# Optimization experiments

Measured on AMD Instinct MI355X. Metric: run time of the kernel, lower is better.

## Reference

```python
import jax, jax.numpy as jnp
import numpy as np

COMMIT_LAMBDA = 0.25


def setup_inputs() -> dict:
    key = jax.random.key(0)
    k1, k2 = jax.random.split(key)
    B, C, T = 8, 256, 1024
    NCB, K, D = 2, 8192, 128
    x = jax.random.normal(k1, (B, C, T), dtype=jnp.float32)
    # EMA codebook weights buffer (init: randn * 0.1)
    codebooks = jax.random.normal(k2, (NCB, K, D), dtype=jnp.float32) * 0.1
    return {"x": x, "codebooks": codebooks}


def reference(x, codebooks):
    B, C, T = x.shape
    ncb, K, d = codebooks.shape
    # [B, C, T] -> [B*T, ncb, d]
    xs = x.reshape(B, ncb, d, T).transpose(0, 3, 1, 2).reshape(B * T, ncb, d)
    # squared euclidean distances (argmin-equivalent to cdist)
    x2 = jnp.sum(xs * xs, axis=-1)[..., None]            # [N, ncb, 1]
    c2 = jnp.sum(codebooks * codebooks, axis=-1)[None]    # [1, ncb, K]
    xc = jnp.einsum('bnd,nkd->bnk', xs, codebooks)        # [N, ncb, K]
    d2 = x2 - 2.0 * xc + c2
    idx = jnp.argmin(d2, axis=-1)                         # [N, ncb] int
    # gather nearest code vectors: [N, ncb, d]
    q = codebooks[jnp.arange(ncb)[None, :], idx]
    # straight-through estimator
    q_st = xs + jax.lax.stop_gradient(q - xs)
    # commitment loss (training mode): sum over codebooks of mse(x_i, q_i.detach())
    loss = COMMIT_LAMBDA * jnp.sum(
        jnp.mean((xs - jax.lax.stop_gradient(q)) ** 2, axis=(0, 2))
    )
    # reassemble to [B, C, T]
    quantized = q_st.reshape(B, T, ncb, d).transpose(0, 2, 3, 1).reshape(B, C, T)
    indices = idx.reshape(B, T, ncb).transpose(0, 2, 1)   # [B, ncb, T]
    return quantized, indices, loss
```

## Files before the change

### kernel.cpp

```cpp
#include <hip/hip_runtime.h>
#include <hip/hip_bf16.h>

#define BB   8
#define TT   1024
#define NCBN 2
#define DD   128
#define KK   8192
#define MM   8192

constexpr int OUT_IDX_OFF  = BB * 256 * TT;
constexpr int OUT_LOSS_OFF = OUT_IDX_OFF + BB * NCBN * TT;

#define THR   0.45f
#define QCAP  768

typedef __attribute__((ext_vector_type(8))) short   short8;
typedef __attribute__((ext_vector_type(4))) float   float4v;

__device__ __forceinline__ unsigned short f2bf(float v) {
    unsigned u = __float_as_uint(v);
    return (unsigned short)((u + 0x7FFFu + ((u >> 16) & 1u)) >> 16);
}

__device__ __forceinline__ void gl_lds16(const void* g, void* l) {
    __builtin_amdgcn_global_load_lds(
        (const __attribute__((address_space(1))) unsigned int*)g,
        (__attribute__((address_space(3))) unsigned int*)l, 16, 0, 0);
}

__global__ __launch_bounds__(256)
void pack_x_kernel(const float* __restrict__ x, unsigned short* __restrict__ xbf,
                   float* __restrict__ x2, unsigned long long* __restrict__ pmin) {
    __shared__ float Ld[DD][65];
    const int b = blockIdx.x >> 1, n = blockIdx.x & 1;
    const int t0 = blockIdx.y * 64;
    const int tid = threadIdx.x;

    const float* base = x + ((size_t)(b * 256 + n * 128)) * TT + t0;
    const int dro = tid >> 2, q4 = tid & 3;
#pragma unroll
    for (int half = 0; half < 2; ++half) {
        int d = dro + half * 64;
        const float* rp = base + (size_t)d * TT + q4 * 16;
#pragma unroll
        for (int j = 0; j < 4; ++j) {
            float4 v = *(const float4*)(rp + j * 4);
            int t = q4 * 16 + j * 4;
            Ld[d][t + 0] = v.x; Ld[d][t + 1] = v.y;
            Ld[d][t + 2] = v.z; Ld[d][t + 3] = v.w;
        }
    }
    __syncthreads();

    if (tid < 64) {
        float s = 0.f;
        for (int d = 0; d < DD; ++d) { float v = Ld[d][tid]; s = fmaf(v, v, s); }
        x2[(size_t)n * MM + b * TT + t0 + tid] = s;
        pmin[(size_t)n * MM + b * TT + t0 + tid] = 0xFFFFFFFFFFFFFFFFull;
    }

    unsigned short* orow0 = xbf + ((size_t)n * MM + b * TT + t0) * DD;
#pragma unroll
    for (int pp = 0; pp < 4; ++pp) {
        int u = tid + pp * 256;
        int tt = u >> 4, sg = u & 15;
        unsigned short tmp[8];
#pragma unroll
        for (int j = 0; j < 8; ++j) tmp[j] = f2bf(Ld[sg * 8 + j][tt]);
        uint4 pk;
        pk.x = (unsigned)tmp[0] | ((unsigned)tmp[1] << 16);
        pk.y = (unsigned)tmp[2] | ((unsigned)tmp[3] << 16);
        pk.z = (unsigned)tmp[4] | ((unsigned)tmp[5] << 16);
        pk.w = (unsigned)tmp[6] | ((unsigned)tmp[7] << 16);
        *(uint4*)(orow0 + (size_t)tt * DD + sg * 8) = pk;
    }
}

__global__ __launch_bounds__(256)
void pack_c_kernel(const float* __restrict__ cb, unsigned short* __restrict__ cbf,
                   float* __restrict__ c2, float* __restrict__ out) {
    int g = blockIdx.x * 256 + threadIdx.x;
    if (g == 0) out[OUT_LOSS_OFF] = 0.f;
    const float4* crow = (const float4*)(cb + (size_t)g * DD);
    unsigned short* orow = cbf + (size_t)g * DD;
    float s = 0.f;
#pragma unroll 4
    for (int i2 = 0; i2 < 16; ++i2) {
        float4 v0 = crow[2 * i2];
        float4 v1 = crow[2 * i2 + 1];
        s = fmaf(v0.x, v0.x, s); s = fmaf(v0.y, v0.y, s);
        s = fmaf(v0.z, v0.z, s); s = fmaf(v0.w, v0.w, s);
        s = fmaf(v1.x, v1.x, s); s = fmaf(v1.y, v1.y, s);
        s = fmaf(v1.z, v1.z, s); s = fmaf(v1.w, v1.w, s);
        uint4 pk;
        pk.x = (unsigned)f2bf(v0.x) | ((unsigned)f2bf(v0.y) << 16);
        pk.y = (unsigned)f2bf(v0.z) | ((unsigned)f2bf(v0.w) << 16);
        pk.z = (unsigned)f2bf(v1.x) | ((unsigned)f2bf(v1.y) << 16);
        pk.w = (unsigned)f2bf(v1.z) | ((unsigned)f2bf(v1.w) << 16);
        *(uint4*)(orow + i2 * 8) = pk;
    }
    c2[g] = s;
}

__device__ void rescore_one(int n, int m, int k,
                            const float* __restrict__ x, const float* __restrict__ cb,
                            const float* __restrict__ x2, const float* __restrict__ c2,
                            unsigned long long* __restrict__ pmin) {
    int b = m >> 10, t = m & (TT - 1);
    const float* xp = x + ((size_t)(b * 256 + n * 128)) * TT + t;
    const float* cp = cb + ((size_t)(n * KK + k)) * DD;
    float xc = 0.f;
    for (int d = 0; d < DD; ++d)
        xc = fmaf(xp[(size_t)d * TT], cp[d], xc);
    float u = x2[n * MM + m] - 2.0f * xc;
    float s = u + c2[n * KK + k];
    unsigned long long pk = ((unsigned long long)__float_as_uint(s) << 32) | (unsigned)k;
    atomicMin(pmin + (size_t)n * MM + m, pk);
}

__global__ __launch_bounds__(256, 2)
void screen_kernel(const unsigned short* __restrict__ xbf,
                   const unsigned short* __restrict__ cbf,
                   const float* __restrict__ c2,
                   const float* __restrict__ x,
                   const float* __restrict__ cb32,
                   const float* __restrict__ x2,
                   unsigned long long* __restrict__ pmin) {
    __shared__ __align__(16) unsigned short Qsh[128 * 128];
    __shared__ __align__(16) unsigned short Ash[128 * 128];
    __shared__ unsigned int   minU[128];
    __shared__ float          c2s[128];
    __shared__ unsigned int   qcnt;
    __shared__ unsigned int   queue[QCAP];

    const int tid = threadIdx.x;
    const int id  = blockIdx.x;
    const int n   = id & 1;
    const int ks  = (id >> 1) & 3;
    const int qt  = id >> 3;
    const int m0  = qt * 128;
    const int k0  = ks * 2048;

    const int wave = tid >> 6, lane = tid & 63;
    const int cw = wave & 1, qw = wave >> 1;
    const int quad = lane >> 4, l15 = lane & 15;

    int goff[8];
#pragma unroll
    for (int p = 0; p < 8; ++p) {
        int u   = (p * 4 + wave) * 64 + lane;
        int row = u >> 4;
        int seg = (u & 15) ^ (row & 15);
        goff[p] = (row * DD + seg * 8) * 2;
    }

    {
        const char* src = (const char*)(xbf + ((size_t)n * MM + m0) * DD);
#pragma unroll
        for (int p = 0; p < 8; ++p)
            gl_lds16(src + goff[p], &Qsh[(p * 4 + wave) * 512]);
    }
    if (tid < 128) minU[tid] = 0xFFFFFFFFu;
    if (tid == 0)  qcnt = 0;
    __syncthreads();

    short8 bfr[4][4];
#pragma unroll
    for (int tq = 0; tq < 4; ++tq) {
        int q = qw * 64 + tq * 16 + l15;
#pragma unroll
        for (int k4 = 0; k4 < 4; ++k4) {
            int seg = k4 * 4 + quad;
            bfr[tq][k4] = *(const short8*)(&Qsh[q * 128 + ((seg ^ l15) * 8)]);
        }
    }

    float mloc[4] = {3.4e38f, 3.4e38f, 3.4e38f, 3.4e38f};
    float thr[4]  = {3.4e38f, 3.4e38f, 3.4e38f, 3.4e38f};

    const char*  asrc0 = (const char*)(cbf + ((size_t)n * KK + k0) * DD);
    const float* c2p   = c2 + (size_t)n * KK + k0;

#pragma unroll
    for (int phase = 0; phase < 2; ++phase) {
        for (int ch = 0; ch < 16; ++ch) {
            __syncthreads();
            {
                const char* src = asrc0 + (size_t)ch * (128 * DD * 2);
#pragma unroll
                for (int p = 0; p < 8; ++p)
                    gl_lds16(src + goff[p], &Ash[(p * 4 + wave) * 512]);
                if (tid < 32)
                    *(float4*)&c2s[tid * 4] =
                        *(const float4*)(c2p + ch * 128 + tid * 4);
            }
            __syncthreads();

            float4v acc[4][4];
#pragma unroll
            for (int tc = 0; tc < 4; ++tc)
#pragma unroll
                for (int tq = 0; tq < 4; ++tq)
                    acc[tc][tq] = (float4v){0.f, 0.f, 0.f, 0.f};

#pragma unroll
            for (int k4 = 0; k4 < 4; ++k4) {
                short8 a[4];
#pragma unroll
                for (int tc = 0; tc < 4; ++tc) {
                    int r = cw * 64 + tc * 16 + l15;
                    int seg = k4 * 4 + quad;
                    a[tc] = *(const short8*)(&Ash[r * 128 + ((seg ^ l15) * 8)]);
                }
#pragma unroll
                for (int tc = 0; tc < 4; ++tc)
#pragma unroll
                    for (int tq = 0; tq < 4; ++tq)
                        acc[tc][tq] = __builtin_amdgcn_mfma_f32_16x16x32_bf16(
                            a[tc], bfr[tq][k4], acc[tc][tq], 0, 0, 0);
            }

#pragma unroll
            for (int tc = 0; tc < 4; ++tc) {
                float4v c2r = *(const float4v*)(&c2s[cw * 64 + tc * 16 + quad * 4]);
#pragma unroll
                for (int tq = 0; tq < 4; ++tq) {
                    float y0 = fmaf(-2.0f, acc[tc][tq][0], c2r[0]);
                    float y1 = fmaf(-2.0f, acc[tc][tq][1], c2r[1]);
                    float y2 = fmaf(-2.0f, acc[tc][tq][2], c2r[2]);
                    float y3 = fmaf(-2.0f, acc[tc][tq][3], c2r[3]);
                    float m4 = fminf(fminf(y0, y1), fminf(y2, y3));
                    if (phase == 0) {
                        mloc[tq] = fminf(mloc[tq], m4);
                    } else if (m4 <= thr[tq]) {
                        float yv[4] = {y0, y1, y2, y3};
#pragma unroll
                        for (int rg = 0; rg < 4; ++rg) {
                            if (yv[rg] <= thr[tq]) {
                                unsigned idx  = atomicAdd(&qcnt, 1u);
                                unsigned code = (unsigned)(ch * 128 + cw * 64 + tc * 16 + quad * 4 + rg);
                                unsigned q    = (unsigned)(qw * 64 + tq * 16 + l15);
                                if (idx < QCAP) queue[idx] = (q << 11) | code;
                                else rescore_one(n, m0 + (int)q, k0 + (int)code,
                                                 x, cb32, x2, c2, pmin);
                            }
                        }
                    }
                }
            }
        }

        if (phase == 0) {
#pragma unroll
            for (int tq = 0; tq < 4; ++tq) {
                float v = mloc[tq];
                v = fminf(v, __shfl_xor(v, 16, 64));
                v = fminf(v, __shfl_xor(v, 32, 64));
                if (quad == 0) {
                    unsigned u  = __float_as_uint(v);
                    unsigned mu = (u & 0x80000000u) ? ~u : (u | 0x80000000u);
                    atomicMin(&minU[qw * 64 + tq * 16 + l15], mu);
                }
            }
            __syncthreads();
#pragma unroll
            for (int tq = 0; tq < 4; ++tq) {
                unsigned mu = minU[qw * 64 + tq * 16 + l15];
                unsigned u  = (mu & 0x80000000u) ? (mu & 0x7FFFFFFFu) : ~mu;
                thr[tq] = __uint_as_float(u) + THR;
            }
        }
    }

    __syncthreads();
    unsigned total = qcnt; if (total > QCAP) total = QCAP;
    for (unsigned i = tid; i < total; i += 256) {
        unsigned ent = queue[i];
        rescore_one(n, m0 + (int)(ent >> 11), k0 + (int)(ent & 2047u),
                    x, cb32, x2, c2, pmin);
    }
}

__global__ __launch_bounds__(256)
void gather_kernel(const float* __restrict__ x, const float* __restrict__ cb,
                   const unsigned long long* __restrict__ pmin,
                   float* __restrict__ out) {
    __shared__ float Cr[64][DD + 1];
    __shared__ int   kid[64];
    const int b = blockIdx.x >> 1, n = blockIdx.x & 1;
    const int t0 = blockIdx.y * 64;
    const int tid = threadIdx.x;

    if (tid < 64) {
        int t = t0 + tid;
        int k = (int)(pmin[(size_t)n * MM + b * TT + t] & 0xFFFFFFFFull);
        kid[tid] = k;
        out[OUT_IDX_OFF + (b * NCBN + n) * TT + t] = (float)k;
    }
    __syncthreads();

    {
        int row = tid >> 2, q4 = tid & 3;
        const float* cp = cb + ((size_t)n * KK + kid[row]) * DD + q4 * 32;
#pragma unroll
        for (int j = 0; j < 8; ++j) {
            float4 v = *(const float4*)(cp + j * 4);
            int d = q4 * 32 + j * 4;
            Cr[row][d + 0] = v.x; Cr[row][d + 1] = v.y;
            Cr[row][d + 2] = v.z; Cr[row][d + 3] = v.w;
        }
    }
    __syncthreads();

    float lsum = 0.f;
    const float* xb = x  + ((size_t)(b * 256 + n * 128)) * TT + t0;
    float*       ob = out + ((size_t)(b * 256 + n * 128)) * TT + t0;
#pragma unroll
    for (int pp = 0; pp < 8; ++pp) {
        int u  = tid + pp * 256;
        int d  = u >> 4, ts = (u & 15) * 4;
        float4 xv = *(const float4*)(xb + (size_t)d * TT + ts);
        float4 qv = { Cr[ts + 0][d], Cr[ts + 1][d], Cr[ts + 2][d], Cr[ts + 3][d] };
        *(float4*)(ob + (size_t)d * TT + ts) = qv;
        float e;
        e = xv.x - qv.x; lsum = fmaf(e, e, lsum);
        e = xv.y - qv.y; lsum = fmaf(e, e, lsum);
        e = xv.z - qv.z; lsum = fmaf(e, e, lsum);
        e = xv.w - qv.w; lsum = fmaf(e, e, lsum);
    }

#pragma unroll
    for (int o = 32; o > 0; o >>= 1) lsum += __shfl_down(lsum, o, 64);
    __shared__ float wsum[4];
    int lane = tid & 63, w = tid >> 6;
    if (lane == 0) wsum[w] = lsum;
    __syncthreads();
    if (tid == 0) {
        float tot = wsum[0] + wsum[1] + wsum[2] + wsum[3];
        atomicAdd(out + OUT_LOSS_OFF, tot * 2.384185791015625e-7f);
    }
}

extern "C" void kernel_launch(void* const* d_in, const int* in_sizes, int n_in,
                              void* d_out, int out_size, void* d_ws, size_t ws_size,
                              hipStream_t stream) {
    (void)in_sizes; (void)n_in; (void)out_size; (void)ws_size;
    const float* x  = (const float*)d_in[0];
    const float* cb = (const float*)d_in[1];
    float* out = (float*)d_out;

    char* ws = (char*)d_ws;
    unsigned short* xbf = (unsigned short*)(ws);
    unsigned short* cbf = (unsigned short*)(ws + (4u << 20));
    float* x2 = (float*)(ws + (8u << 20));
    float* c2 = (float*)(ws + (8u << 20) + (64u << 10));
    unsigned long long* pmin =
        (unsigned long long*)(ws + (8u << 20) + (128u << 10));

    pack_x_kernel<<<dim3(16, 16), 256, 0, stream>>>(x, xbf, x2, pmin);
    pack_c_kernel<<<dim3(64), 256, 0, stream>>>(cb, cbf, c2, out);

    screen_kernel<<<dim3(512), 256, 0, stream>>>(xbf, cbf, c2, x, cb, x2, pmin);
    gather_kernel<<<dim3(16, 16), 256, 0, stream>>>(x, cb, pmin, out);
}
```

Before: 184.3 us.

## Replace two-pass screening with single-pass running-threshold screen and double-buffered codebook tiles

The screening kernel used to sweep all 16 codebook chunks twice: once to find each query's minimum, then again to enqueue candidates within a margin. It now sweeps once, using a running per-query minimum as the threshold, and re-checks chunk 0 at the end because its threshold was not yet known when it was first scored. Codebook chunks are double-buffered in LDS so the next chunk's load overlaps the current MFMA work, and the single barrier per chunk replaces two. A looser running threshold can enqueue more candidates, so the queue capacity grows, which uses more LDS and may lower occupancy.

```diff
diff --git a/kernel.cpp b/kernel.cpp
--- a/kernel.cpp
+++ b/kernel.cpp
@@ -12,7 +12,7 @@
 constexpr int OUT_LOSS_OFF = OUT_IDX_OFF + BB * NCBN * TT;
 
 #define THR   0.45f
-#define QCAP  768
+#define QCAP  2048
 
 typedef __attribute__((ext_vector_type(8))) short   short8;
 typedef __attribute__((ext_vector_type(4))) float   float4v;
@@ -126,10 +126,9 @@
                    const float* __restrict__ cb32,
                    const float* __restrict__ x2,
                    unsigned long long* __restrict__ pmin) {
-    __shared__ __align__(16) unsigned short Qsh[128 * 128];
-    __shared__ __align__(16) unsigned short Ash[128 * 128];
+    __shared__ __align__(16) unsigned short Csh[2][128 * 128];
+    __shared__ float          c2s[2][128];
     __shared__ unsigned int   minU[128];
-    __shared__ float          c2s[128];
     __shared__ unsigned int   qcnt;
     __shared__ unsigned int   queue[QCAP];
 
@@ -154,12 +153,19 @@
         goff[p] = (row * DD + seg * 8) * 2;
     }
 
+    const char*  asrc0 = (const char*)(cbf + ((size_t)n * KK + k0) * DD);
+    const float* c2p   = c2 + (size_t)n * KK + k0;
+
     {
-        const char* src = (const char*)(xbf + ((size_t)n * MM + m0) * DD);
+        const char* qsrc = (const char*)(xbf + ((size_t)n * MM + m0) * DD);
 #pragma unroll
         for (int p = 0; p < 8; ++p)
-            gl_lds16(src + goff[p], &Qsh[(p * 4 + wave) * 512]);
-    }
+            gl_lds16(qsrc + goff[p], &Csh[0][(p * 4 + wave) * 512]);
+#pragma unroll
+        for (int p = 0; p < 8; ++p)
+            gl_lds16(asrc0 + goff[p], &Csh[1][(p * 4 + wave) * 512]);
+    }
+    if (tid < 32)  *(float4*)&c2s[1][tid * 4] = *(const float4*)(c2p + tid * 4);
     if (tid < 128) minU[tid] = 0xFFFFFFFFu;
     if (tid == 0)  qcnt = 0;
     __syncthreads();
@@ -171,74 +177,93 @@
 #pragma unroll
         for (int k4 = 0; k4 < 4; ++k4) {
             int seg = k4 * 4 + quad;
-            bfr[tq][k4] = *(const short8*)(&Qsh[q * 128 + ((seg ^ l15) * 8)]);
-        }
-    }
-
-    float mloc[4] = {3.4e38f, 3.4e38f, 3.4e38f, 3.4e38f};
-    float thr[4]  = {3.4e38f, 3.4e38f, 3.4e38f, 3.4e38f};
-
-    const char*  asrc0 = (const char*)(cbf + ((size_t)n * KK + k0) * DD);
-    const float* c2p   = c2 + (size_t)n * KK + k0;
-
-#pragma unroll
-    for (int phase = 0; phase < 2; ++phase) {
-        for (int ch = 0; ch < 16; ++ch) {
-            __syncthreads();
-            {
-                const char* src = asrc0 + (size_t)ch * (128 * DD * 2);
-#pragma unroll
-                for (int p = 0; p < 8; ++p)
-                    gl_lds16(src + goff[p], &Ash[(p * 4 + wave) * 512]);
-                if (tid < 32)
-                    *(float4*)&c2s[tid * 4] =
-                        *(const float4*)(c2p + ch * 128 + tid * 4);
-            }
-            __syncthreads();
-
-            float4v acc[4][4];
+            bfr[tq][k4] = *(const short8*)(&Csh[0][q * 128 + ((seg ^ l15) * 8)]);
+        }
+    }
+    __syncthreads();
+
+    float thr[4] = {3.4e38f, 3.4e38f, 3.4e38f, 3.4e38f};
+
+    for (int it = 0; it <= 16; ++it) {
+        const int sb   = it & 1;
+        const int cbuf = sb ^ 1;
+        const int dcur = (it < 16) ? it : 0;
+
+        if (it < 16) {
+            const int dn = (it + 1 < 16) ? (it + 1) : 0;
+            const char* src = asrc0 + (size_t)dn * (128 * DD * 2);
+#pragma unroll
+            for (int p = 0; p < 8; ++p)
+                gl_lds16(src + goff[p], &Csh[sb][(p * 4 + wave) * 512]);
+            if (tid < 32)
+                *(float4*)&c2s[sb][tid * 4] =
+                    *(const float4*)(c2p + dn * 128 + tid * 4);
+        }
+
+        float4v acc[4][4];
+#pragma unroll
+        for (int tc = 0; tc < 4; ++tc)
+#pragma unroll
+            for (int tq = 0; tq < 4; ++tq)
+                acc[tc][tq] = (float4v){0.f, 0.f, 0.f, 0.f};
+
+#pragma unroll
+        for (int k4 = 0; k4 < 4; ++k4) {
+            short8 a[4];
+#pragma unroll
+            for (int tc = 0; tc < 4; ++tc) {
+                int r = cw * 64 + tc * 16 + l15;
+                int seg = k4 * 4 + quad;
+                a[tc] = *(const short8*)(&Csh[cbuf][r * 128 + ((seg ^ l15) * 8)]);
+            }
 #pragma unroll
             for (int tc = 0; tc < 4; ++tc)
 #pragma unroll
                 for (int tq = 0; tq < 4; ++tq)
-                    acc[tc][tq] = (float4v){0.f, 0.f, 0.f, 0.f};
-
-#pragma unroll
-            for (int k4 = 0; k4 < 4; ++k4) {
-                short8 a[4];
-#pragma unroll
-                for (int tc = 0; tc < 4; ++tc) {
-                    int r = cw * 64 + tc * 16 + l15;
-                    int seg = k4 * 4 + quad;
-                    a[tc] = *(const short8*)(&Ash[r * 128 + ((seg ^ l15) * 8)]);
-                }
-#pragma unroll
-                for (int tc = 0; tc < 4; ++tc)
-#pragma unroll
-                    for (int tq = 0; tq < 4; ++tq)
-                        acc[tc][tq] = __builtin_amdgcn_mfma_f32_16x16x32_bf16(
-                            a[tc], bfr[tq][k4], acc[tc][tq], 0, 0, 0);
-            }
-
+                    acc[tc][tq] = __builtin_amdgcn_mfma_f32_16x16x32_bf16(
+                        a[tc], bfr[tq][k4], acc[tc][tq], 0, 0, 0);
+        }
+
+        float cmin[4] = {3.4e38f, 3.4e38f, 3.4e38f, 3.4e38f};
+#pragma unroll
+        for (int tc = 0; tc < 4; ++tc) {
+            float4v c2r = *(const float4v*)(&c2s[cbuf][cw * 64 + tc * 16 + quad * 4]);
+#pragma unroll
+            for (int tq = 0; tq < 4; ++tq) {
+                float y0 = fmaf(-2.0f, acc[tc][tq][0], c2r[0]);
+                float y1 = fmaf(-2.0f, acc[tc][tq][1], c2r[1]);
+                float y2 = fmaf(-2.0f, acc[tc][tq][2], c2r[2]);
+                float y3 = fmaf(-2.0f, acc[tc][tq][3], c2r[3]);
+                acc[tc][tq] = (float4v){y0, y1, y2, y3};
+                cmin[tq] = fminf(cmin[tq],
+                                 fminf(fminf(y0, y1), fminf(y2, y3)));
+            }
+        }
+#pragma unroll
+        for (int tq = 0; tq < 4; ++tq) {
+            float v = cmin[tq];
+            v = fminf(v, __shfl_xor(v, 16, 64));
+            v = fminf(v, __shfl_xor(v, 32, 64));
+            cmin[tq] = v;
+        }
+
+        if (it > 0) {
+            float te[4];
+#pragma unroll
+            for (int tq = 0; tq < 4; ++tq)
+                te[tq] = fminf(thr[tq], cmin[tq] + THR);
 #pragma unroll
             for (int tc = 0; tc < 4; ++tc) {
-                float4v c2r = *(const float4v*)(&c2s[cw * 64 + tc * 16 + quad * 4]);
 #pragma unroll
                 for (int tq = 0; tq < 4; ++tq) {
-                    float y0 = fmaf(-2.0f, acc[tc][tq][0], c2r[0]);
-                    float y1 = fmaf(-2.0f, acc[tc][tq][1], c2r[1]);
-                    float y2 = fmaf(-2.0f, acc[tc][tq][2], c2r[2]);
-                    float y3 = fmaf(-2.0f, acc[tc][tq][3], c2r[3]);
-                    float m4 = fminf(fminf(y0, y1), fminf(y2, y3));
-                    if (phase == 0) {
-                        mloc[tq] = fminf(mloc[tq], m4);
-                    } else if (m4 <= thr[tq]) {
-                        float yv[4] = {y0, y1, y2, y3};
+                    float4v yv = acc[tc][tq];
+                    float m4 = fminf(fminf(yv[0], yv[1]), fminf(yv[2], yv[3]));
+                    if (m4 <= te[tq]) {
 #pragma unroll
                         for (int rg = 0; rg < 4; ++rg) {
-                            if (yv[rg] <= thr[tq]) {
+                            if (yv[rg] <= te[tq]) {
                                 unsigned idx  = atomicAdd(&qcnt, 1u);
-                                unsigned code = (unsigned)(ch * 128 + cw * 64 + tc * 16 + quad * 4 + rg);
+                                unsigned code = (unsigned)(dcur * 128 + cw * 64 + tc * 16 + quad * 4 + rg);
                                 unsigned q    = (unsigned)(qw * 64 + tq * 16 + l15);
                                 if (idx < QCAP) queue[idx] = (q << 11) | code;
                                 else rescore_one(n, m0 + (int)q, k0 + (int)code,
@@ -250,19 +275,16 @@
             }
         }
 
-        if (phase == 0) {
-#pragma unroll
-            for (int tq = 0; tq < 4; ++tq) {
-                float v = mloc[tq];
-                v = fminf(v, __shfl_xor(v, 16, 64));
-                v = fminf(v, __shfl_xor(v, 32, 64));
-                if (quad == 0) {
-                    unsigned u  = __float_as_uint(v);
-                    unsigned mu = (u & 0x80000000u) ? ~u : (u | 0x80000000u);
-                    atomicMin(&minU[qw * 64 + tq * 16 + l15], mu);
-                }
-            }
-            __syncthreads();
+#pragma unroll
+        for (int tq = 0; tq < 4; ++tq) {
+            if (quad == 0) {
+                unsigned u  = __float_as_uint(cmin[tq]);
+                unsigned mu = (u & 0x80000000u) ? ~u : (u | 0x80000000u);
+                atomicMin(&minU[qw * 64 + tq * 16 + l15], mu);
+            }
+        }
+        __syncthreads();
+        if (it < 16) {
 #pragma unroll
             for (int tq = 0; tq < 4; ++tq) {
                 unsigned mu = minU[qw * 64 + tq * 16 + l15];
@@ -272,7 +294,6 @@
         }
     }
 
-    __syncthreads();
     unsigned total = qcnt; if (total > QCAP) total = QCAP;
     for (unsigned i = tid; i < total; i += 256) {
         unsigned ent = queue[i];
```

Result: slower. 208.7 us (+13.3%).
